# Kernel optimization log

Measured on AMD Instinct MI355X. Metric: run time of the kernel, lower is better.

## Reference

```python
import jax, jax.numpy as jnp
import numpy as np

N = 8192   # nodes
M = 8192   # hyperedges
B = 32     # batch
S = 12     # input_dim (time steps / features)
D = 12     # out_dim
H = 8      # heads
NNZ = 262144  # nonzeros in hg (avg degree 32)
ALPHA = 0.2   # leaky relu slope
NEG = -1000000000.0


def _leaky(x):
    return jax.nn.leaky_relu(x, ALPHA)


def setup_inputs() -> dict:
    rng = np.random.default_rng(0)
    flat = np.sort(rng.choice(N * M, size=NNZ, replace=False))
    idx0 = (flat // M).astype(np.int32)  # node index of each incidence
    idx1 = (flat % M).astype(np.int32)   # hyperedge index
    hg = np.zeros((N, M), np.float32)
    hg[idx0, idx1] = 1.0

    key = jax.random.key(0)
    ks = jax.random.split(key, 9)
    sc = 0.3  # xavier-ish scale for 12-dim fan
    return {
        "x": jax.random.normal(ks[0], (B, S, N), jnp.float32),
        "hg": jnp.asarray(hg),
        "idx0": jnp.asarray(idx0),
        "idx1": jnp.asarray(idx1),
        "P": jax.random.normal(ks[1], (S, D), jnp.float32) * sc,
        "W0": jax.random.normal(ks[2], (H, S, D), jnp.float32) * sc,
        "A": jax.random.normal(ks[3], (H, 2 * D), jnp.float32) * sc,
        "W2": jax.random.normal(ks[4], (H, D, D), jnp.float32) * sc,
        "lin_w": jax.random.normal(ks[5], (1, H), jnp.float32) * sc,
        "lin_b": jax.random.normal(ks[6], (1,), jnp.float32) * 0.01,
        "gcn_w": jax.random.normal(ks[7], (D, D), jnp.float32) * sc,
        "gcn_b": jax.random.normal(ks[8], (D,), jnp.float32) * 0.01,
    }


def reference(x, hg, idx0, idx1, P, W0, A, W2, lin_w, lin_b, gcn_w, gcn_b):
    xp = jnp.transpose(x, (0, 2, 1))                    # [B, N, S]
    xP = jnp.einsum('bns,sd->bnd', xp, P)               # [B, N, D]
    e = _leaky(jnp.einsum('nm,bnd->bmd', hg, xP))       # hg.T @ xP -> [B, M, D]

    # Per-head edge attention; torch code only uses batch index 0.
    x0 = xp[0]                                          # [N, S]
    e0 = e[0]                                           # [M, D]
    x_h = jnp.einsum('ns,hsd->hnd', x0, W0)             # [H, N, D]
    e_h = jnp.einsum('md,hdk->hmk', e0, W2)             # [H, M, D]
    a1, a2 = A[:, :D], A[:, D:]                         # split a = [a1 | a2]
    ax = jnp.einsum('hnd,hd->hn', x_h, a1)              # [H, N]
    ae = jnp.einsum('hmd,hd->hm', e_h, a2)              # [H, M]
    atts = _leaky(ax[:, idx0] + ae[:, idx1])            # [H, NNZ]

    # linear over heads: [NNZ, H] @ w.T + b
    mt = jnp.einsum('hz,h->z', atts, lin_w[0]) + lin_b[0]  # [NNZ]

    mask = jnp.where(hg == 0, NEG, 0.0).astype(x.dtype)
    dense = jnp.zeros((N, M), x.dtype).at[idx0, idx1].set(mt) + mask
    att = jax.nn.softmax(dense, axis=1)                 # [N, M]

    occ = jnp.einsum('nm,bmd->bnd', att, e)             # [B, N, D]
    y = _leaky(occ @ gcn_w.T + gcn_b)                   # dropout p=0 -> identity
    return y
```

## Files before the change

### kernel.cpp

```cpp
#include <hip/hip_runtime.h>

namespace {

constexpr int N    = 8192;
constexpr int M    = 8192;
constexpr int B    = 32;
constexpr int S    = 12;
constexpr int D    = 12;
constexpr int H    = 8;
constexpr int NNZ  = 262144;
constexpr float ALPHA = 0.2f;
constexpr int BD   = B * D;
constexpr int BD2  = BD / 2;
constexpr int RU4  = BD / 8;
constexpr int CSC_CAP = 128;
constexpr int CPB  = 8;

__device__ __forceinline__ float leaky(float v) { return v >= 0.0f ? v : ALPHA * v; }

__device__ __forceinline__ float blo(unsigned v) { return __uint_as_float(v << 16); }
__device__ __forceinline__ float bhi(unsigned v) { return __uint_as_float(v & 0xffff0000u); }
__device__ __forceinline__ unsigned bpack(float a, float b) {
  unsigned x = __float_as_uint(a), y = __float_as_uint(b);
  x = (x + 0x7fffu + ((x >> 16) & 1u)) >> 16;
  y = (y + 0x7fffu + ((y >> 16) & 1u)) & 0xffff0000u;
  return x | y;
}

__global__ void k_prep(const float* __restrict__ x, const float* __restrict__ P,
                       const float* __restrict__ W0, const float* __restrict__ A,
                       const int* __restrict__ idx0, unsigned* __restrict__ xPt_u,
                       float* __restrict__ ax, int* __restrict__ row_ptr,
                       int* __restrict__ colfill) {
  __shared__ float w0a_s[H * S];
  int t = blockIdx.x * blockDim.x + threadIdx.x;
  if (blockIdx.x < 32 && threadIdx.x < H * S) {
    int h = threadIdx.x / S;
    float a = 0.f;
#pragma unroll
    for (int d = 0; d < D; ++d) a += W0[threadIdx.x * D + d] * A[h * 2 * D + d];
    w0a_s[threadIdx.x] = a;
  }
  if (t < M) colfill[t] = 0;
  if (t <= N) {
    int lo = 0, hi = NNZ;
    while (lo < hi) {
      int mid = (lo + hi) >> 1;
      if (idx0[mid] < t) lo = mid + 1; else hi = mid;
    }
    row_ptr[t] = lo;
  }
  if (blockIdx.x < 32) __syncthreads();
  if (t >= B * N) return;
  int b = t >> 13, n = t & (N - 1);
  float xv[S];
#pragma unroll
  for (int s = 0; s < S; ++s) xv[s] = x[((size_t)b * S + s) * N + n];
  float a[D];
#pragma unroll
  for (int d = 0; d < D; ++d) {
    float acc = 0.f;
#pragma unroll
    for (int s = 0; s < S; ++s) acc += xv[s] * P[s * D + d];
    a[d] = acc;
  }
#pragma unroll
  for (int i = 0; i < D / 2; ++i)
    xPt_u[(size_t)n * BD2 + b * (D / 2) + i] = bpack(a[2 * i], a[2 * i + 1]);
  if (b == 0) {
#pragma unroll
    for (int h = 0; h < H; ++h) {
      float acc = 0.f;
#pragma unroll
      for (int s = 0; s < S; ++s) acc += xv[s] * w0a_s[h * S + s];
      ax[n * H + h] = acc;
    }
  }
}

__global__ void k_fill_csc(const int* __restrict__ idx0, const int* __restrict__ idx1,
                           int* __restrict__ colfill, int* __restrict__ csc_rows) {
  int z = blockIdx.x * blockDim.x + threadIdx.x;
  if (z >= NNZ) return;
  int c = idx1[z];
  int p = atomicAdd(&colfill[c], 1);
  if (p < CSC_CAP) csc_rows[c * CSC_CAP + p] = idx0[z];
}

__global__ void k_e(const uint4* __restrict__ xPt4, const int* __restrict__ colfill,
                    const int* __restrict__ csc_rows, const float* __restrict__ W2,
                    const float* __restrict__ A, uint4* __restrict__ e4,
                    float* __restrict__ ae) {
  int tid = threadIdx.x;
  int col = tid / RU4, lt = tid - col * RU4;
  int m = blockIdx.x * CPB + col;
  __shared__ int rows[CPB][CSC_CAP];
  __shared__ float w2a_s[H * D];
  __shared__ float e0_s[CPB][D];
  int cnt = min(colfill[m], CSC_CAP);
  for (int j = lt; j < cnt; j += RU4) rows[col][j] = csc_rows[m * CSC_CAP + j];
  if (tid < H * D) {
    int h = tid / D;
    float a = 0.f;
#pragma unroll
    for (int k = 0; k < D; ++k) a += W2[tid * D + k] * A[h * 2 * D + D + k];
    w2a_s[tid] = a;
  }
  __syncthreads();
  float a[8] = {0.f, 0.f, 0.f, 0.f, 0.f, 0.f, 0.f, 0.f};
  for (int j = 0; j < cnt; ++j) {
    uint4 v = xPt4[(size_t)rows[col][j] * RU4 + lt];
    a[0] += blo(v.x); a[1] += bhi(v.x);
    a[2] += blo(v.y); a[3] += bhi(v.y);
    a[4] += blo(v.z); a[5] += bhi(v.z);
    a[6] += blo(v.w); a[7] += bhi(v.w);
  }
#pragma unroll
  for (int k = 0; k < 8; ++k) a[k] = leaky(a[k]);
  uint4 o;
  o.x = bpack(a[0], a[1]); o.y = bpack(a[2], a[3]);
  o.z = bpack(a[4], a[5]); o.w = bpack(a[6], a[7]);
  e4[(size_t)m * RU4 + lt] = o;
  if (lt == 0) {
#pragma unroll
    for (int k = 0; k < 8; ++k) e0_s[col][k] = a[k];
  } else if (lt == 1) {
#pragma unroll
    for (int k = 0; k < 4; ++k) e0_s[col][8 + k] = a[k];
  }
  __syncthreads();
  if (tid < CPB * H) {
    int c = tid / H, h = tid - c * H;
    float s = 0.f;
#pragma unroll
    for (int d = 0; d < D; ++d) s += e0_s[c][d] * w2a_s[h * D + d];
    ae[(blockIdx.x * CPB + c) * H + h] = s;
  }
}

__global__ void k_wgt(const int* __restrict__ idx1, const int* __restrict__ row_ptr,
                      const float* __restrict__ ax, const float* __restrict__ ae,
                      const float* __restrict__ lin_w, const float* __restrict__ lin_b,
                      float* __restrict__ wgt) {
  int warp = threadIdx.x >> 6, lane = threadIdx.x & 63;
  int n = blockIdx.x * 4 + warp;
  int beg = row_ptr[n], end = row_ptr[n + 1], cnt = end - beg;
  if (cnt <= 0) return;
  float axv[H], lw[H];
#pragma unroll
  for (int h = 0; h < H; ++h) { axv[h] = ax[n * H + h]; lw[h] = lin_w[h]; }
  float lb = lin_b[0];
  float mt0 = -3.0e38f, mt1 = -3.0e38f;
  int j0 = lane, j1 = lane + 64;
  if (j0 < cnt) {
    int mm = idx1[beg + j0];
    float mv = lb;
#pragma unroll
    for (int h = 0; h < H; ++h) mv += lw[h] * leaky(axv[h] + ae[mm * H + h]);
    mt0 = mv;
  }
  if (j1 < cnt) {
    int mm = idx1[beg + j1];
    float mv = lb;
#pragma unroll
    for (int h = 0; h < H; ++h) mv += lw[h] * leaky(axv[h] + ae[mm * H + h]);
    mt1 = mv;
  }
  float mx = fmaxf(mt0, mt1);
#pragma unroll
  for (int off = 32; off; off >>= 1) mx = fmaxf(mx, __shfl_xor(mx, off));
  float p0 = (j0 < cnt) ? expf(mt0 - mx) : 0.f;
  float p1 = (j1 < cnt) ? expf(mt1 - mx) : 0.f;
  float sum = p0 + p1;
#pragma unroll
  for (int off = 32; off; off >>= 1) sum += __shfl_xor(sum, off);
  float inv = 1.0f / sum;
  if (j0 < cnt) wgt[beg + j0] = p0 * inv;
  if (j1 < cnt) wgt[beg + j1] = p1 * inv;
}

__global__ void k_y(const int* __restrict__ idx1, const int* __restrict__ row_ptr,
                    const float* __restrict__ wgt, const uint4* __restrict__ e4,
                    const float* __restrict__ gcn_w, const float* __restrict__ gcn_b,
                    float* __restrict__ y) {
  int tid = threadIdx.x;
  int col = tid / RU4, lt = tid - col * RU4;
  int n = blockIdx.x * CPB + col;
  __shared__ int idx_s[CPB][CSC_CAP];
  __shared__ float w_s[CPB][CSC_CAP];
  __shared__ float gw_s[D * D];
  __shared__ float gb_s[D];
  __shared__ float occ_s[CPB][BD];
  int beg = row_ptr[n], end = row_ptr[n + 1];
  int cnt = min(end - beg, CSC_CAP);
  for (int j = lt; j < cnt; j += RU4) {
    idx_s[col][j] = idx1[beg + j];
    w_s[col][j] = wgt[beg + j];
  }
  if (tid < D * D) gw_s[tid] = gcn_w[tid];
  if (tid >= 256 && tid < 256 + D) gb_s[tid - 256] = gcn_b[tid - 256];
  __syncthreads();
  float a[8] = {0.f, 0.f, 0.f, 0.f, 0.f, 0.f, 0.f, 0.f};
  if (cnt > 0) {
    for (int j = 0; j < cnt; ++j) {
      uint4 v = e4[(size_t)idx_s[col][j] * RU4 + lt];
      float w = w_s[col][j];
      a[0] += w * blo(v.x); a[1] += w * bhi(v.x);
      a[2] += w * blo(v.y); a[3] += w * bhi(v.y);
      a[4] += w * blo(v.z); a[5] += w * bhi(v.z);
      a[6] += w * blo(v.w); a[7] += w * bhi(v.w);
    }
  } else {
    for (int mm = 0; mm < M; ++mm) {
      uint4 v = e4[(size_t)mm * RU4 + lt];
      a[0] += blo(v.x); a[1] += bhi(v.x);
      a[2] += blo(v.y); a[3] += bhi(v.y);
      a[4] += blo(v.z); a[5] += bhi(v.z);
      a[6] += blo(v.w); a[7] += bhi(v.w);
    }
#pragma unroll
    for (int k = 0; k < 8; ++k) a[k] *= (1.0f / (float)M);
  }
#pragma unroll
  for (int k = 0; k < 8; ++k) occ_s[col][8 * lt + k] = a[k];
  __syncthreads();
  int b = tid / D, d = tid - b * D;
#pragma unroll
  for (int c = 0; c < CPB; ++c) {
    float s = gb_s[d];
#pragma unroll
    for (int k = 0; k < D; ++k) s += occ_s[c][b * D + k] * gw_s[d * D + k];
    y[(size_t)b * N * D + (size_t)(blockIdx.x * CPB + c) * D + d] = leaky(s);
  }
}

}

extern "C" void kernel_launch(void* const* d_in, const int* in_sizes, int n_in,
                              void* d_out, int out_size, void* d_ws, size_t ws_size,
                              hipStream_t stream) {
  const float* x     = (const float*)d_in[0];
  const int*   idx0  = (const int*)d_in[2];
  const int*   idx1  = (const int*)d_in[3];
  const float* P     = (const float*)d_in[4];
  const float* W0    = (const float*)d_in[5];
  const float* A     = (const float*)d_in[6];
  const float* W2    = (const float*)d_in[7];
  const float* lin_w = (const float*)d_in[8];
  const float* lin_b = (const float*)d_in[9];
  const float* gcn_w = (const float*)d_in[10];
  const float* gcn_b = (const float*)d_in[11];
  float* y = (float*)d_out;

  char* ws = (char*)d_ws;
  size_t off = 0;
  auto carve = [&](size_t bytes) {
    char* p = ws + off;
    off = (off + bytes + 255) & ~(size_t)255;
    return p;
  };
  unsigned* xPt_u   = (unsigned*)carve(sizeof(unsigned) * (size_t)N * BD2);
  unsigned* e_u     = (unsigned*)carve(sizeof(unsigned) * (size_t)M * BD2);
  float*    ax      = (float*)carve(sizeof(float) * N * H);
  float*    ae      = (float*)carve(sizeof(float) * M * H);
  float*    wgt     = (float*)carve(sizeof(float) * NNZ);
  int*      colfill = (int*)carve(sizeof(int) * M);
  int*      row_ptr = (int*)carve(sizeof(int) * (N + 1));
  int*      csc_rows= (int*)carve(sizeof(int) * (size_t)M * CSC_CAP);
  (void)ws_size; (void)in_sizes; (void)n_in; (void)out_size;

  k_prep<<<(B * N + 255) / 256, 256, 0, stream>>>(x, P, W0, A, idx0, xPt_u, ax,
                                                  row_ptr, colfill);
  k_fill_csc<<<(NNZ + 255) / 256, 256, 0, stream>>>(idx0, idx1, colfill, csc_rows);
  k_e<<<M / CPB, 384, 0, stream>>>((const uint4*)xPt_u, colfill, csc_rows, W2, A,
                                   (uint4*)e_u, ae);
  k_wgt<<<N / 4, 256, 0, stream>>>(idx1, row_ptr, ax, ae, lin_w, lin_b, wgt);
  k_y<<<N / CPB, 384, 0, stream>>>(idx1, row_ptr, wgt, (const uint4*)e_u,
                                   gcn_w, gcn_b, y);
}
```

Baseline: 69.43 us.

## Split batch into two halves for gather kernels to shrink working set

Result: slower. 76.67 us (+10.4%).

```diff
diff --git a/kernel.cpp b/kernel.cpp
--- a/kernel.cpp
+++ b/kernel.cpp
@@ -11,10 +11,10 @@
 constexpr int NNZ  = 262144;
 constexpr float ALPHA = 0.2f;
 constexpr int BD   = B * D;
-constexpr int BD2  = BD / 2;
-constexpr int RU4  = BD / 8;
+constexpr int HB2  = BD / 2 / 2;
+constexpr int HU4  = HB2 / 4;
 constexpr int CSC_CAP = 128;
-constexpr int CPB  = 8;
+constexpr int CPB  = 16;
 
 __device__ __forceinline__ float leaky(float v) { return v >= 0.0f ? v : ALPHA * v; }
 
@@ -64,9 +64,11 @@
     for (int s = 0; s < S; ++s) acc += xv[s] * P[s * D + d];
     a[d] = acc;
   }
+  int half = b >> 4, bl = b & 15;
 #pragma unroll
   for (int i = 0; i < D / 2; ++i)
-    xPt_u[(size_t)n * BD2 + b * (D / 2) + i] = bpack(a[2 * i], a[2 * i + 1]);
+    xPt_u[(size_t)half * N * HB2 + (size_t)n * HB2 + bl * (D / 2) + i] =
+        bpack(a[2 * i], a[2 * i + 1]);
   if (b == 0) {
 #pragma unroll
     for (int h = 0; h < H; ++h) {
@@ -90,16 +92,17 @@
 __global__ void k_e(const uint4* __restrict__ xPt4, const int* __restrict__ colfill,
                     const int* __restrict__ csc_rows, const float* __restrict__ W2,
                     const float* __restrict__ A, uint4* __restrict__ e4,
-                    float* __restrict__ ae) {
+                    float* __restrict__ ae, int half) {
   int tid = threadIdx.x;
-  int col = tid / RU4, lt = tid - col * RU4;
+  int col = tid / HU4, lt = tid - col * HU4;
   int m = blockIdx.x * CPB + col;
   __shared__ int rows[CPB][CSC_CAP];
   __shared__ float w2a_s[H * D];
   __shared__ float e0_s[CPB][D];
+  const uint4* src = xPt4 + (size_t)half * N * HU4;
   int cnt = min(colfill[m], CSC_CAP);
-  for (int j = lt; j < cnt; j += RU4) rows[col][j] = csc_rows[m * CSC_CAP + j];
-  if (tid < H * D) {
+  for (int j = lt; j < cnt; j += HU4) rows[col][j] = csc_rows[m * CSC_CAP + j];
+  if (half == 0 && tid < H * D) {
     int h = tid / D;
     float a = 0.f;
 #pragma unroll
@@ -109,7 +112,7 @@
   __syncthreads();
   float a[8] = {0.f, 0.f, 0.f, 0.f, 0.f, 0.f, 0.f, 0.f};
   for (int j = 0; j < cnt; ++j) {
-    uint4 v = xPt4[(size_t)rows[col][j] * RU4 + lt];
+    uint4 v = src[(size_t)rows[col][j] * HU4 + lt];
     a[0] += blo(v.x); a[1] += bhi(v.x);
     a[2] += blo(v.y); a[3] += bhi(v.y);
     a[4] += blo(v.z); a[5] += bhi(v.z);
@@ -120,21 +123,23 @@
   uint4 o;
   o.x = bpack(a[0], a[1]); o.y = bpack(a[2], a[3]);
   o.z = bpack(a[4], a[5]); o.w = bpack(a[6], a[7]);
-  e4[(size_t)m * RU4 + lt] = o;
-  if (lt == 0) {
-#pragma unroll
-    for (int k = 0; k < 8; ++k) e0_s[col][k] = a[k];
-  } else if (lt == 1) {
-#pragma unroll
-    for (int k = 0; k < 4; ++k) e0_s[col][8 + k] = a[k];
-  }
-  __syncthreads();
-  if (tid < CPB * H) {
-    int c = tid / H, h = tid - c * H;
-    float s = 0.f;
-#pragma unroll
-    for (int d = 0; d < D; ++d) s += e0_s[c][d] * w2a_s[h * D + d];
-    ae[(blockIdx.x * CPB + c) * H + h] = s;
+  e4[(size_t)half * M * HU4 + (size_t)m * HU4 + lt] = o;
+  if (half == 0) {
+    if (lt == 0) {
+#pragma unroll
+      for (int k = 0; k < 8; ++k) e0_s[col][k] = a[k];
+    } else if (lt == 1) {
+#pragma unroll
+      for (int k = 0; k < 4; ++k) e0_s[col][8 + k] = a[k];
+    }
+    __syncthreads();
+    if (tid < CPB * H) {
+      int c = tid / H, h = tid - c * H;
+      float s = 0.f;
+#pragma unroll
+      for (int d = 0; d < D; ++d) s += e0_s[c][d] * w2a_s[h * D + d];
+      ae[(blockIdx.x * CPB + c) * H + h] = s;
+    }
   }
 }
 
@@ -182,18 +187,19 @@
 __global__ void k_y(const int* __restrict__ idx1, const int* __restrict__ row_ptr,
                     const float* __restrict__ wgt, const uint4* __restrict__ e4,
                     const float* __restrict__ gcn_w, const float* __restrict__ gcn_b,
-                    float* __restrict__ y) {
+                    float* __restrict__ y, int half) {
   int tid = threadIdx.x;
-  int col = tid / RU4, lt = tid - col * RU4;
+  int col = tid / HU4, lt = tid - col * HU4;
   int n = blockIdx.x * CPB + col;
   __shared__ int idx_s[CPB][CSC_CAP];
   __shared__ float w_s[CPB][CSC_CAP];
   __shared__ float gw_s[D * D];
   __shared__ float gb_s[D];
-  __shared__ float occ_s[CPB][BD];
+  __shared__ float occ_s[CPB][2 * HB2];
+  const uint4* src = e4 + (size_t)half * M * HU4;
   int beg = row_ptr[n], end = row_ptr[n + 1];
   int cnt = min(end - beg, CSC_CAP);
-  for (int j = lt; j < cnt; j += RU4) {
+  for (int j = lt; j < cnt; j += HU4) {
     idx_s[col][j] = idx1[beg + j];
     w_s[col][j] = wgt[beg + j];
   }
@@ -203,7 +209,7 @@
   float a[8] = {0.f, 0.f, 0.f, 0.f, 0.f, 0.f, 0.f, 0.f};
   if (cnt > 0) {
     for (int j = 0; j < cnt; ++j) {
-      uint4 v = e4[(size_t)idx_s[col][j] * RU4 + lt];
+      uint4 v = src[(size_t)idx_s[col][j] * HU4 + lt];
       float w = w_s[col][j];
       a[0] += w * blo(v.x); a[1] += w * bhi(v.x);
       a[2] += w * blo(v.y); a[3] += w * bhi(v.y);
@@ -212,7 +218,7 @@
     }
   } else {
     for (int mm = 0; mm < M; ++mm) {
-      uint4 v = e4[(size_t)mm * RU4 + lt];
+      uint4 v = src[(size_t)mm * HU4 + lt];
       a[0] += blo(v.x); a[1] += bhi(v.x);
       a[2] += blo(v.y); a[3] += bhi(v.y);
       a[4] += blo(v.z); a[5] += bhi(v.z);
@@ -224,12 +230,13 @@
 #pragma unroll
   for (int k = 0; k < 8; ++k) occ_s[col][8 * lt + k] = a[k];
   __syncthreads();
-  int b = tid / D, d = tid - b * D;
-#pragma unroll
-  for (int c = 0; c < CPB; ++c) {
+  int e2 = tid % (2 * HB2), rr = tid / (2 * HB2);
+  int b_local = e2 / D, d = e2 - b_local * D;
+  int b = half * 16 + b_local;
+  for (int c = rr; c < CPB; c += 2) {
     float s = gb_s[d];
 #pragma unroll
-    for (int k = 0; k < D; ++k) s += occ_s[c][b * D + k] * gw_s[d * D + k];
+    for (int k = 0; k < D; ++k) s += occ_s[c][b_local * D + k] * gw_s[d * D + k];
     y[(size_t)b * N * D + (size_t)(blockIdx.x * CPB + c) * D + d] = leaky(s);
   }
 }
@@ -259,8 +266,8 @@
     off = (off + bytes + 255) & ~(size_t)255;
     return p;
   };
-  unsigned* xPt_u   = (unsigned*)carve(sizeof(unsigned) * (size_t)N * BD2);
-  unsigned* e_u     = (unsigned*)carve(sizeof(unsigned) * (size_t)M * BD2);
+  unsigned* xPt_u   = (unsigned*)carve(sizeof(unsigned) * (size_t)2 * N * HB2);
+  unsigned* e_u     = (unsigned*)carve(sizeof(unsigned) * (size_t)2 * M * HB2);
   float*    ax      = (float*)carve(sizeof(float) * N * H);
   float*    ae      = (float*)carve(sizeof(float) * M * H);
   float*    wgt     = (float*)carve(sizeof(float) * NNZ);
@@ -273,8 +280,12 @@
                                                   row_ptr, colfill);
   k_fill_csc<<<(NNZ + 255) / 256, 256, 0, stream>>>(idx0, idx1, colfill, csc_rows);
   k_e<<<M / CPB, 384, 0, stream>>>((const uint4*)xPt_u, colfill, csc_rows, W2, A,
-                                   (uint4*)e_u, ae);
+                                   (uint4*)e_u, ae, 0);
+  k_e<<<M / CPB, 384, 0, stream>>>((const uint4*)xPt_u, colfill, csc_rows, W2, A,
+                                   (uint4*)e_u, ae, 1);
   k_wgt<<<N / 4, 256, 0, stream>>>(idx1, row_ptr, ax, ae, lin_w, lin_b, wgt);
   k_y<<<N / CPB, 384, 0, stream>>>(idx1, row_ptr, wgt, (const uint4*)e_u,
-                                   gcn_w, gcn_b, y);
-}
+                                   gcn_w, gcn_b, y, 0);
+  k_y<<<N / CPB, 384, 0, stream>>>(idx1, row_ptr, wgt, (const uint4*)e_u,
+                                   gcn_w, gcn_b, y, 1);
+}
```

## Fuse attention-weight softmax into aggregation kernel and use nontemporal stores

Applied to the files above, without the earlier changes.

Result: slower. 83.12 us (+19.7%).

```diff
diff --git a/kernel.cpp b/kernel.cpp
--- a/kernel.cpp
+++ b/kernel.cpp
@@ -16,6 +16,8 @@
 constexpr int CSC_CAP = 128;
 constexpr int CPB  = 8;
 
+using uv4 = __attribute__((ext_vector_type(4))) unsigned int;
+
 __device__ __forceinline__ float leaky(float v) { return v >= 0.0f ? v : ALPHA * v; }
 
 __device__ __forceinline__ float blo(unsigned v) { return __uint_as_float(v << 16); }
@@ -66,7 +68,8 @@
   }
 #pragma unroll
   for (int i = 0; i < D / 2; ++i)
-    xPt_u[(size_t)n * BD2 + b * (D / 2) + i] = bpack(a[2 * i], a[2 * i + 1]);
+    __builtin_nontemporal_store(bpack(a[2 * i], a[2 * i + 1]),
+                                &xPt_u[(size_t)n * BD2 + b * (D / 2) + i]);
   if (b == 0) {
 #pragma unroll
     for (int h = 0; h < H; ++h) {
@@ -84,7 +87,7 @@
   if (z >= NNZ) return;
   int c = idx1[z];
   int p = atomicAdd(&colfill[c], 1);
-  if (p < CSC_CAP) csc_rows[c * CSC_CAP + p] = idx0[z];
+  if (p < CSC_CAP) __builtin_nontemporal_store(idx0[z], &csc_rows[c * CSC_CAP + p]);
 }
 
 __global__ void k_e(const uint4* __restrict__ xPt4, const int* __restrict__ colfill,
@@ -117,10 +120,10 @@
   }
 #pragma unroll
   for (int k = 0; k < 8; ++k) a[k] = leaky(a[k]);
-  uint4 o;
+  uv4 o;
   o.x = bpack(a[0], a[1]); o.y = bpack(a[2], a[3]);
   o.z = bpack(a[4], a[5]); o.w = bpack(a[6], a[7]);
-  e4[(size_t)m * RU4 + lt] = o;
+  __builtin_nontemporal_store(o, (uv4*)&e4[(size_t)m * RU4 + lt]);
   if (lt == 0) {
 #pragma unroll
     for (int k = 0; k < 8; ++k) e0_s[col][k] = a[k];
@@ -138,73 +141,79 @@
   }
 }
 
-__global__ void k_wgt(const int* __restrict__ idx1, const int* __restrict__ row_ptr,
-                      const float* __restrict__ ax, const float* __restrict__ ae,
-                      const float* __restrict__ lin_w, const float* __restrict__ lin_b,
-                      float* __restrict__ wgt) {
-  int warp = threadIdx.x >> 6, lane = threadIdx.x & 63;
-  int n = blockIdx.x * 4 + warp;
-  int beg = row_ptr[n], end = row_ptr[n + 1], cnt = end - beg;
-  if (cnt <= 0) return;
-  float axv[H], lw[H];
-#pragma unroll
-  for (int h = 0; h < H; ++h) { axv[h] = ax[n * H + h]; lw[h] = lin_w[h]; }
-  float lb = lin_b[0];
-  float mt0 = -3.0e38f, mt1 = -3.0e38f;
-  int j0 = lane, j1 = lane + 64;
-  if (j0 < cnt) {
-    int mm = idx1[beg + j0];
-    float mv = lb;
-#pragma unroll
-    for (int h = 0; h < H; ++h) mv += lw[h] * leaky(axv[h] + ae[mm * H + h]);
-    mt0 = mv;
-  }
-  if (j1 < cnt) {
-    int mm = idx1[beg + j1];
-    float mv = lb;
-#pragma unroll
-    for (int h = 0; h < H; ++h) mv += lw[h] * leaky(axv[h] + ae[mm * H + h]);
-    mt1 = mv;
-  }
-  float mx = fmaxf(mt0, mt1);
-#pragma unroll
-  for (int off = 32; off; off >>= 1) mx = fmaxf(mx, __shfl_xor(mx, off));
-  float p0 = (j0 < cnt) ? expf(mt0 - mx) : 0.f;
-  float p1 = (j1 < cnt) ? expf(mt1 - mx) : 0.f;
-  float sum = p0 + p1;
-#pragma unroll
-  for (int off = 32; off; off >>= 1) sum += __shfl_xor(sum, off);
-  float inv = 1.0f / sum;
-  if (j0 < cnt) wgt[beg + j0] = p0 * inv;
-  if (j1 < cnt) wgt[beg + j1] = p1 * inv;
-}
-
-__global__ void k_y(const int* __restrict__ idx1, const int* __restrict__ row_ptr,
-                    const float* __restrict__ wgt, const uint4* __restrict__ e4,
-                    const float* __restrict__ gcn_w, const float* __restrict__ gcn_b,
-                    float* __restrict__ y) {
+__global__ void k_yw(const int* __restrict__ idx1, const int* __restrict__ row_ptr,
+                     const float* __restrict__ ax, const float* __restrict__ ae,
+                     const float* __restrict__ lin_w, const float* __restrict__ lin_b,
+                     const uint4* __restrict__ e4, const float* __restrict__ gcn_w,
+                     const float* __restrict__ gcn_b, float* __restrict__ y) {
   int tid = threadIdx.x;
   int col = tid / RU4, lt = tid - col * RU4;
-  int n = blockIdx.x * CPB + col;
-  __shared__ int idx_s[CPB][CSC_CAP];
-  __shared__ float w_s[CPB][CSC_CAP];
+  int n0 = blockIdx.x * CPB;
   __shared__ float gw_s[D * D];
   __shared__ float gb_s[D];
+  __shared__ float ax_s[CPB][H];
+  __shared__ float lw_s[H];
+  __shared__ float lb_s;
+  __shared__ int   beg_s[CPB];
+  __shared__ int   cnt_s[CPB];
+  __shared__ int   idx_s[CPB][CSC_CAP];
+  __shared__ float mt_s[CPB][CSC_CAP];
   __shared__ float occ_s[CPB][BD];
-  int beg = row_ptr[n], end = row_ptr[n + 1];
-  int cnt = min(end - beg, CSC_CAP);
-  for (int j = lt; j < cnt; j += RU4) {
-    idx_s[col][j] = idx1[beg + j];
-    w_s[col][j] = wgt[beg + j];
-  }
+
   if (tid < D * D) gw_s[tid] = gcn_w[tid];
-  if (tid >= 256 && tid < 256 + D) gb_s[tid - 256] = gcn_b[tid - 256];
+  if (tid >= 144 && tid < 144 + D) gb_s[tid - 144] = gcn_b[tid - 144];
+  if (tid >= 192 && tid < 192 + CPB * H) {
+    int u = tid - 192, r = u >> 3, h = u & 7;
+    ax_s[r][h] = ax[(n0 + r) * H + h];
+  }
+  if (tid >= 256 && tid < 256 + H) lw_s[tid - 256] = lin_w[tid - 256];
+  if (tid == 256 + H) lb_s = lin_b[0];
+  if (tid < CPB) {
+    int b = row_ptr[n0 + tid];
+    beg_s[tid] = b;
+    cnt_s[tid] = min(row_ptr[n0 + tid + 1] - b, CSC_CAP);
+  }
+  __syncthreads();
+  for (int j = lt; j < cnt_s[col]; j += RU4) idx_s[col][j] = idx1[beg_s[col] + j];
+  __syncthreads();
+  for (int j0 = tid; j0 < CPB * CSC_CAP; j0 += 384) {
+    int r = j0 >> 7, jj = j0 & (CSC_CAP - 1);
+    if (jj < cnt_s[r]) {
+      int mm = idx_s[r][jj];
+      float mv = lb_s;
+#pragma unroll
+      for (int h = 0; h < H; ++h) mv += lw_s[h] * leaky(ax_s[r][h] + ae[mm * H + h]);
+      mt_s[r][jj] = mv;
+    }
+  }
+  __syncthreads();
+  {
+    int w = tid >> 6, lane = tid & 63;
+    for (int r = w; r < CPB; r += 6) {
+      int cnt = cnt_s[r];
+      if (cnt <= 0) continue;
+      float m0 = (lane < cnt) ? mt_s[r][lane] : -3.0e38f;
+      float m1 = (lane + 64 < cnt) ? mt_s[r][lane + 64] : -3.0e38f;
+      float mx = fmaxf(m0, m1);
+#pragma unroll
+      for (int off = 32; off; off >>= 1) mx = fmaxf(mx, __shfl_xor(mx, off));
+      float p0 = (lane < cnt) ? expf(m0 - mx) : 0.f;
+      float p1 = (lane + 64 < cnt) ? expf(m1 - mx) : 0.f;
+      float sum = p0 + p1;
+#pragma unroll
+      for (int off = 32; off; off >>= 1) sum += __shfl_xor(sum, off);
+      float inv = 1.0f / sum;
+      if (lane < cnt) mt_s[r][lane] = p0 * inv;
+      if (lane + 64 < cnt) mt_s[r][lane + 64] = p1 * inv;
+    }
+  }
   __syncthreads();
   float a[8] = {0.f, 0.f, 0.f, 0.f, 0.f, 0.f, 0.f, 0.f};
+  int cnt = cnt_s[col];
   if (cnt > 0) {
     for (int j = 0; j < cnt; ++j) {
       uint4 v = e4[(size_t)idx_s[col][j] * RU4 + lt];
-      float w = w_s[col][j];
+      float w = mt_s[col][j];
       a[0] += w * blo(v.x); a[1] += w * bhi(v.x);
       a[2] += w * blo(v.y); a[3] += w * bhi(v.y);
       a[4] += w * blo(v.z); a[5] += w * bhi(v.z);
@@ -230,7 +239,8 @@
     float s = gb_s[d];
 #pragma unroll
     for (int k = 0; k < D; ++k) s += occ_s[c][b * D + k] * gw_s[d * D + k];
-    y[(size_t)b * N * D + (size_t)(blockIdx.x * CPB + c) * D + d] = leaky(s);
+    __builtin_nontemporal_store(leaky(s),
+        &y[(size_t)b * N * D + (size_t)(n0 + c) * D + d]);
   }
 }
 
@@ -263,7 +273,6 @@
   unsigned* e_u     = (unsigned*)carve(sizeof(unsigned) * (size_t)M * BD2);
   float*    ax      = (float*)carve(sizeof(float) * N * H);
   float*    ae      = (float*)carve(sizeof(float) * M * H);
-  float*    wgt     = (float*)carve(sizeof(float) * NNZ);
   int*      colfill = (int*)carve(sizeof(int) * M);
   int*      row_ptr = (int*)carve(sizeof(int) * (N + 1));
   int*      csc_rows= (int*)carve(sizeof(int) * (size_t)M * CSC_CAP);
@@ -274,7 +283,6 @@
   k_fill_csc<<<(NNZ + 255) / 256, 256, 0, stream>>>(idx0, idx1, colfill, csc_rows);
   k_e<<<M / CPB, 384, 0, stream>>>((const uint4*)xPt_u, colfill, csc_rows, W2, A,
                                    (uint4*)e_u, ae);
-  k_wgt<<<N / 4, 256, 0, stream>>>(idx1, row_ptr, ax, ae, lin_w, lin_b, wgt);
-  k_y<<<N / CPB, 384, 0, stream>>>(idx1, row_ptr, wgt, (const uint4*)e_u,
-                                   gcn_w, gcn_b, y);
-}
+  k_yw<<<N / CPB, 384, 0, stream>>>(idx1, row_ptr, ax, ae, lin_w, lin_b,
+                                    (const uint4*)e_u, gcn_w, gcn_b, y);
+}
```
